# Kernel optimization log

Measured on AMD Instinct MI355X. Metric: run time of the kernel, lower is better.

Reference implementation:

```python
import jax, jax.numpy as jnp
import numpy as np
import math

B, N, D, H = 4, 2048, 256, 4
DH = D // H
EPS = 1e-8


def setup_inputs() -> dict:
    key = jax.random.key(0)
    ks = jax.random.split(key, 8)
    x = jax.random.normal(ks[0], (B, N, D), dtype=jnp.float32)
    # RoPE rotation freqs: exp(i * pos * inv_freq), stored as (cos, sin) pairs -> [N, DH//2, 2]
    d2 = DH // 2
    inv_freq = 1.0 / (10000.0 ** (jnp.arange(d2, dtype=jnp.float32) / d2))
    ang = jnp.arange(N, dtype=jnp.float32)[:, None] * inv_freq[None, :]
    freqs = jnp.stack([jnp.cos(ang), jnp.sin(ang)], axis=-1)  # [N, d2, 2]
    s = 0.02
    g = jnp.ones((D,), dtype=jnp.float32)
    w_qkv = jax.random.normal(ks[1], (D, 3 * D), dtype=jnp.float32) * s
    b_qkv = jnp.zeros((3 * D,), dtype=jnp.float32)
    w_out = jax.random.normal(ks[2], (D, D), dtype=jnp.float32) * s
    b_out = jnp.zeros((D,), dtype=jnp.float32)
    w_gate = jax.random.normal(ks[3], (D, D), dtype=jnp.float32) * s
    b_gate = jnp.zeros((D,), dtype=jnp.float32)
    return {"x": x, "freqs": freqs, "g": g, "w_qkv": w_qkv, "b_qkv": b_qkv,
            "w_out": w_out, "b_out": b_out, "w_gate": w_gate, "b_gate": b_gate}


def _zcrmsnorm(x, g):
    x0 = x - jnp.mean(x, axis=-1, keepdims=True)
    rms = jnp.sqrt(jnp.mean(x0 * x0, axis=-1, keepdims=True) + EPS)
    return x0 / rms * g


def _rope(q, freqs):
    # q: [B,H,N,DH]; freqs: [N,DH//2,2] (cos,sin). Complex multiply on adjacent pairs.
    b, h, n, dh = q.shape
    qp = q.reshape(b, h, n, dh // 2, 2)
    cos = freqs[:n, :, 0][None, None]  # [1,1,N,d2]
    sin = freqs[:n, :, 1][None, None]
    q0, q1 = qp[..., 0], qp[..., 1]
    out = jnp.stack([q0 * cos - q1 * sin, q0 * sin + q1 * cos], axis=-1)
    return out.reshape(b, h, n, dh)


def reference(x, freqs, g, w_qkv, b_qkv, w_out, b_out, w_gate, b_gate):
    b, n, d = x.shape
    h = _zcrmsnorm(x, g)
    qkv = (h @ w_qkv + b_qkv).reshape(b, n, 3, H, DH)
    qkv = jnp.transpose(qkv, (2, 0, 3, 1, 4))  # [3,B,H,N,DH]
    q, k, v = qkv[0], qkv[1], qkv[2]
    q = _rope(q, freqs)
    k = _rope(k, freqs)
    scores = jnp.einsum('bhqd,bhkd->bhqk', q, k) / math.sqrt(DH)
    attn = jax.nn.softmax(scores, axis=-1)  # dropout is identity in eval
    y = jnp.einsum('bhqk,bhkd->bhqd', attn, v)
    y = jnp.transpose(y, (0, 2, 1, 3)).reshape(b, n, d)
    y = y @ w_out + b_out
    gate = jax.nn.sigmoid(h @ w_gate + b_gate)
    return x + gate * y
```

## Files before the change

kernel.cpp:

```cpp
#include <hip/hip_runtime.h>

typedef unsigned short u16;
typedef unsigned int u32;
typedef short short8 __attribute__((ext_vector_type(8)));
typedef float f32x4 __attribute__((ext_vector_type(4)));
typedef float f32x16 __attribute__((ext_vector_type(16)));

#define B_ 4
#define N_ 2048
#define D_ 256
#define H_ 4
#define DH_ 64
#define BN_ 8192

__device__ inline float b2f(u16 u) {
    union { u32 i; float f; } v; v.i = ((u32)u) << 16; return v.f;
}
__device__ inline u16 f2b(float f) {
    union { float f; u32 i; } v; v.f = f;
    return (u16)((v.i + 0x8000u) >> 16);
}
__device__ inline u32 pkbf(float a, float b) {
    union { float f; u32 i; } ua, ub; ua.f = a; ub.f = b;
    return __builtin_amdgcn_perm(ub.i + 0x8000u, ua.i + 0x8000u, 0x07060302u);
}
__device__ inline f32x4 mfma16(short8 a, short8 b, f32x4 c) {
    return __builtin_amdgcn_mfma_f32_16x16x32_bf16(a, b, c, 0, 0, 0);
}
__device__ inline f32x16 mfma32(short8 a, short8 b, f32x16 c) {
    return __builtin_amdgcn_mfma_f32_32x32x16_bf16(a, b, c, 0, 0, 0);
}

__device__ __forceinline__ void gemm_body(
    int bx, int by, int tid,
    const u16* __restrict__ A, const u16* __restrict__ BT,
    const float* __restrict__ bias, void* __restrict__ Cout,
    int Ntot)
{
    const int wave = tid >> 6, lane = tid & 63;
    const int ln15 = lane & 15, quad = lane >> 4;
    const int m0 = bx * 128 + (wave & 1) * 64;
    const int n0 = by * 128 + (wave >> 1) * 64;

    const f32x4 zero = {0.f, 0.f, 0.f, 0.f};
    f32x4 acc[4][4];
    #pragma unroll
    for (int i = 0; i < 4; ++i)
        #pragma unroll
        for (int j = 0; j < 4; ++j) acc[i][j] = zero;

    #pragma unroll
    for (int k0 = 0; k0 < 256; k0 += 32) {
        const int koff = k0 + quad * 8;
        short8 a[4], b[4];
        #pragma unroll
        for (int i = 0; i < 4; ++i)
            a[i] = *(const short8*)(A + (size_t)(m0 + i * 16 + ln15) * 256 + koff);
        #pragma unroll
        for (int j = 0; j < 4; ++j)
            b[j] = *(const short8*)(BT + (size_t)(n0 + j * 16 + ln15) * 256 + koff);
        #pragma unroll
        for (int i = 0; i < 4; ++i)
            #pragma unroll
            for (int j = 0; j < 4; ++j)
                acc[i][j] = mfma16(a[i], b[j], acc[i][j]);
    }

    #pragma unroll
    for (int i = 0; i < 4; ++i) {
        const int r = m0 + i * 16 + quad * 4;
        #pragma unroll
        for (int j = 0; j < 4; ++j) {
            const int c = n0 + j * 16 + ln15;
            const float bv = bias[c];
            #pragma unroll
            for (int rg = 0; rg < 4; ++rg) {
                const size_t idx = (size_t)(r + rg) * Ntot + c;
                ((u16*)Cout)[idx] = f2b(acc[i][j][rg] + bv);
            }
        }
    }
}

__device__ __forceinline__ void gemm_thin_body(
    int bx, int by, int tid,
    const u16* __restrict__ A, const u16* __restrict__ BT,
    const float* __restrict__ bias, void* __restrict__ Cout,
    const float* __restrict__ xin, const u16* __restrict__ gate,
    int mode)
{
    const int wave = tid >> 6, lane = tid & 63;
    const int ln15 = lane & 15, quad = lane >> 4;
    const int m0 = bx * 64 + (wave & 1) * 32;
    const int n0 = by * 64 + (wave >> 1) * 32;

    const f32x4 zero = {0.f, 0.f, 0.f, 0.f};
    f32x4 acc[2][2];
    #pragma unroll
    for (int i = 0; i < 2; ++i)
        #pragma unroll
        for (int j = 0; j < 2; ++j) acc[i][j] = zero;

    #pragma unroll
    for (int k0 = 0; k0 < 256; k0 += 32) {
        const int koff = k0 + quad * 8;
        short8 a[2], b[2];
        #pragma unroll
        for (int i = 0; i < 2; ++i)
            a[i] = *(const short8*)(A + (size_t)(m0 + i * 16 + ln15) * 256 + koff);
        #pragma unroll
        for (int j = 0; j < 2; ++j)
            b[j] = *(const short8*)(BT + (size_t)(n0 + j * 16 + ln15) * 256 + koff);
        #pragma unroll
        for (int i = 0; i < 2; ++i)
            #pragma unroll
            for (int j = 0; j < 2; ++j)
                acc[i][j] = mfma16(a[i], b[j], acc[i][j]);
    }

    #pragma unroll
    for (int i = 0; i < 2; ++i) {
        const int r = m0 + i * 16 + quad * 4;
        #pragma unroll
        for (int j = 0; j < 2; ++j) {
            const int c = n0 + j * 16 + ln15;
            const float bv = bias[c];
            #pragma unroll
            for (int rg = 0; rg < 4; ++rg) {
                const size_t idx = (size_t)(r + rg) * 256 + c;
                float v = acc[i][j][rg] + bv;
                if (mode == 1) {
                    ((u16*)Cout)[idx] = f2b(1.0f / (1.0f + __expf(-v)));
                } else {
                    ((float*)Cout)[idx] = xin[idx] + b2f(gate[idx]) * v;
                }
            }
        }
    }
}

__global__ __launch_bounds__(256) void gemm_ep(
    const u16* __restrict__ A, const u16* __restrict__ BT,
    const float* __restrict__ bias, void* __restrict__ Cout, int Ntot)
{
    gemm_body(blockIdx.x, blockIdx.y, threadIdx.x, A, BT, bias, Cout, Ntot);
}

__global__ __launch_bounds__(256) void gemm_thin(
    const u16* __restrict__ A, const u16* __restrict__ BT,
    const float* __restrict__ bias, void* __restrict__ Cout,
    const float* __restrict__ xin, const u16* __restrict__ gate, int mode)
{
    gemm_thin_body(blockIdx.x, blockIdx.y, threadIdx.x, A, BT, bias, Cout,
                   xin, gate, mode);
}

__global__ __launch_bounds__(256) void norm_transw_k(
    const float* __restrict__ x, const float* __restrict__ g, u16* __restrict__ h,
    const float* __restrict__ wqkv, const float* __restrict__ wout,
    const float* __restrict__ wgate,
    u16* __restrict__ wqkvT, u16* __restrict__ woutT, u16* __restrict__ wgateT)
{
    if (blockIdx.x < 2048) {
        const int wave = threadIdx.x >> 6, lane = threadIdx.x & 63;
        const int t = blockIdx.x * 4 + wave;
        const float4 u = *(const float4*)(x + (size_t)t * D_ + lane * 4);
        float s  = u.x + u.y + u.z + u.w;
        float s2 = u.x * u.x + u.y * u.y + u.z * u.z + u.w * u.w;
        #pragma unroll
        for (int m = 1; m < 64; m <<= 1) {
            s  += __shfl_xor(s, m);
            s2 += __shfl_xor(s2, m);
        }
        float mean = s * (1.0f / D_);
        float var  = s2 * (1.0f / D_) - mean * mean;
        float rinv = rsqrtf(var + 1e-8f);
        const float4 gv = *(const float4*)(g + lane * 4);
        uint2 o;
        o.x = pkbf((u.x - mean) * rinv * gv.x, (u.y - mean) * rinv * gv.y);
        o.y = pkbf((u.z - mean) * rinv * gv.z, (u.w - mean) * rinv * gv.w);
        *(uint2*)(h + (size_t)t * D_ + lane * 4) = o;
    } else {
        int idx = (blockIdx.x - 2048) * 256 + threadIdx.x;
        if (idx < 768 * 256) {
            int nn = idx >> 8, kk = idx & 255;
            wqkvT[idx] = f2b(wqkv[kk * 768 + nn]);
        }
        idx -= 768 * 256;
        if (idx >= 0 && idx < 256 * 256) {
            int nn = idx >> 8, kk = idx & 255;
            woutT[idx]  = f2b(wout[kk * 256 + nn]);
            wgateT[idx] = f2b(wgate[kk * 256 + nn]);
        }
    }
}

#define QSCALE 0.18033688f
__global__ __launch_bounds__(256) void rope_vt_gate_k(
    const u16* __restrict__ qkv, const float* __restrict__ freqs,
    u16* __restrict__ Q, u16* __restrict__ K, u16* __restrict__ VT,
    const u16* __restrict__ h, const u16* __restrict__ wgateT,
    const float* __restrict__ b_gate, u16* __restrict__ gatb)
{
    __shared__ __align__(16) u16 tile[64 * 65];
    const int blk = blockIdx.x;
    if (blk < 1024) {
        const int idx = blk * 256 + threadIdx.x;
        const int t = idx >> 5, rem = idx & 31;
        const int hh = rem >> 3, s8 = rem & 7;
        const int b = t >> 11, n = t & 2047;

        const float4 f0 = *(const float4*)(freqs + (size_t)n * 64 + s8 * 8);
        const float4 f1 = *(const float4*)(freqs + (size_t)n * 64 + s8 * 8 + 4);

        const u16* qp = qkv + (size_t)t * 768 + hh * 64 + s8 * 8;
        const uint4 qv = *(const uint4*)qp;
        const uint4 kv = *(const uint4*)(qp + 256);

        const size_t off = ((size_t)(b * H_ + hh) * N_ + n) * DH_ + s8 * 8;
        uint4 qo, ko;
        {
            float q0 = b2f((u16)(qv.x & 0xffff)), q1 = b2f((u16)(qv.x >> 16));
            float k0 = b2f((u16)(kv.x & 0xffff)), k1 = b2f((u16)(kv.x >> 16));
            qo.x = pkbf((q0 * f0.x - q1 * f0.y) * QSCALE, (q0 * f0.y + q1 * f0.x) * QSCALE);
            ko.x = pkbf(k0 * f0.x - k1 * f0.y, k0 * f0.y + k1 * f0.x);
        }
        {
            float q0 = b2f((u16)(qv.y & 0xffff)), q1 = b2f((u16)(qv.y >> 16));
            float k0 = b2f((u16)(kv.y & 0xffff)), k1 = b2f((u16)(kv.y >> 16));
            qo.y = pkbf((q0 * f0.z - q1 * f0.w) * QSCALE, (q0 * f0.w + q1 * f0.z) * QSCALE);
            ko.y = pkbf(k0 * f0.z - k1 * f0.w, k0 * f0.w + k1 * f0.z);
        }
        {
            float q0 = b2f((u16)(qv.z & 0xffff)), q1 = b2f((u16)(qv.z >> 16));
            float k0 = b2f((u16)(kv.z & 0xffff)), k1 = b2f((u16)(kv.z >> 16));
            qo.z = pkbf((q0 * f1.x - q1 * f1.y) * QSCALE, (q0 * f1.y + q1 * f1.x) * QSCALE);
            ko.z = pkbf(k0 * f1.x - k1 * f1.y, k0 * f1.y + k1 * f1.x);
        }
        {
            float q0 = b2f((u16)(qv.w & 0xffff)), q1 = b2f((u16)(qv.w >> 16));
            float k0 = b2f((u16)(kv.w & 0xffff)), k1 = b2f((u16)(kv.w >> 16));
            qo.w = pkbf((q0 * f1.z - q1 * f1.w) * QSCALE, (q0 * f1.w + q1 * f1.z) * QSCALE);
            ko.w = pkbf(k0 * f1.z - k1 * f1.w, k0 * f1.w + k1 * f1.z);
        }
        *(uint4*)(Q + off) = qo;
        *(uint4*)(K + off) = ko;
    } else if (blk < 1536) {
        const int id2 = blk - 1024;
        const int bh = id2 & 15;
        const int n0 = (id2 >> 4) * 64;
        const int b = bh >> 2, hh = bh & 3;
        #pragma unroll
        for (int rep = 0; rep < 16; ++rep) {
            int idx = rep * 256 + threadIdx.x;
            int nl = idx >> 6, dh = idx & 63;
            tile[dh * 65 + nl] = qkv[(size_t)(b * N_ + n0 + nl) * 768 + 512 + hh * 64 + dh];
        }
        __syncthreads();
        #pragma unroll
        for (int rep = 0; rep < 16; ++rep) {
            int idx = rep * 256 + threadIdx.x;
            int dh = idx >> 6, nl = idx & 63;
            VT[((size_t)bh * 64 + dh) * N_ + n0 + nl] = tile[dh * 65 + nl];
        }
    } else {
        const int id3 = blk - 1536;
        gemm_thin_body(id3 & 127, id3 >> 7, threadIdx.x, h, wgateT, b_gate,
                       (void*)gatb, (const float*)nullptr, (const u16*)nullptr, 1);
    }
}

__global__ __launch_bounds__(256, 2) void attn_k(
    const u16* __restrict__ Q, const u16* __restrict__ K,
    const u16* __restrict__ VT, float* __restrict__ Op,
    float* __restrict__ lvp)
{
    __shared__ __align__(16) u16 Ks[2][64][64];
    __shared__ __align__(16) u16 Vs[2][64][64];
    const int tid = threadIdx.x;
    const int wave = tid >> 6, lane = tid & 63;
    const int l31 = lane & 31, hi = lane >> 5;
    const int id = blockIdx.x;
    const int bh   = ((id & 7) << 1) | ((id >> 3) & 1);
    const int half = (id >> 4) & 1;
    const int q0   = (id >> 5) * 128 + wave * 32;
    const int kt0  = half * 1024;

    const u16* Qh = Q + (size_t)bh * N_ * DH_;
    const u16* Kh = K + (size_t)bh * N_ * DH_;
    const u16* Vh = VT + (size_t)bh * DH_ * N_;

    short8 bq[4];
    #pragma unroll
    for (int kc = 0; kc < 4; ++kc)
        bq[kc] = *(const short8*)(Qh + (size_t)(q0 + l31) * DH_ + kc * 16 + hi * 8);

    f32x16 o0, o1;
    #pragma unroll
    for (int i = 0; i < 16; ++i) { o0[i] = 0.f; o1[i] = 0.f; }
    float lv = 0.f;

    const int srow = tid >> 2, sq4 = tid & 3;
    const int sw = srow & 7;
    const int wg0 = ((sq4) ^ sw) * 8;
    const int wg1 = ((sq4 + 4) ^ sw) * 8;
    const int rsw = l31 & 7;

    {
        uint4 k0 = *(const uint4*)(Kh + (size_t)(kt0 + srow) * DH_ + sq4 * 8);
        uint4 k1 = *(const uint4*)(Kh + (size_t)(kt0 + srow) * DH_ + (sq4 + 4) * 8);
        uint4 v0 = *(const uint4*)(Vh + (size_t)srow * N_ + kt0 + sq4 * 8);
        uint4 v1 = *(const uint4*)(Vh + (size_t)srow * N_ + kt0 + (sq4 + 4) * 8);
        *(uint4*)&Ks[0][srow][wg0] = k0;
        *(uint4*)&Ks[0][srow][wg1] = k1;
        *(uint4*)&Vs[0][srow][wg0] = v0;
        *(uint4*)&Vs[0][srow][wg1] = v1;
    }
    __syncthreads();

    int p = 0;
    for (int c = 0; c < 16; ++c) {
        const bool more = (c + 1 < 16);
        uint4 k0, k1, v0, v1;
        if (more) {
            const int ktn = kt0 + (c + 1) * 64;
            k0 = *(const uint4*)(Kh + (size_t)(ktn + srow) * DH_ + sq4 * 8);
            k1 = *(const uint4*)(Kh + (size_t)(ktn + srow) * DH_ + (sq4 + 4) * 8);
            v0 = *(const uint4*)(Vh + (size_t)srow * N_ + ktn + sq4 * 8);
            v1 = *(const uint4*)(Vh + (size_t)srow * N_ + ktn + (sq4 + 4) * 8);
        }

        f32x16 st0, st1;
        #pragma unroll
        for (int i = 0; i < 16; ++i) { st0[i] = 0.f; st1[i] = 0.f; }
        #pragma unroll
        for (int kc = 0; kc < 4; ++kc) {
            const int gran = ((2 * kc + hi) ^ rsw) * 8;
            short8 ka0 = *(const short8*)&Ks[p][l31][gran];
            short8 ka1 = *(const short8*)&Ks[p][32 + l31][gran];
            st0 = mfma32(ka0, bq[kc], st0);
            st1 = mfma32(ka1, bq[kc], st1);
        }

        short8 pb[4];
        #pragma unroll
        for (int g = 0; g < 2; ++g) {
            float pr[16];
            #pragma unroll
            for (int r = 0; r < 16; ++r) {
                pr[r] = exp2f(g ? st1[r] : st0[r]);
                lv += pr[r];
            }
            #pragma unroll
            for (int kc2 = 0; kc2 < 2; ++kc2) {
                u32 X0, X1, Y0, Y1;
                asm("v_cvt_pk_bf16_f32 %0, %1, %2" : "=v"(X0) : "v"(pr[8*kc2+0]), "v"(pr[8*kc2+1]));
                asm("v_cvt_pk_bf16_f32 %0, %1, %2" : "=v"(X1) : "v"(pr[8*kc2+2]), "v"(pr[8*kc2+3]));
                asm("v_cvt_pk_bf16_f32 %0, %1, %2" : "=v"(Y0) : "v"(pr[8*kc2+4]), "v"(pr[8*kc2+5]));
                asm("v_cvt_pk_bf16_f32 %0, %1, %2" : "=v"(Y1) : "v"(pr[8*kc2+6]), "v"(pr[8*kc2+7]));
                asm("v_permlane32_swap_b32 %0, %1" : "+v"(X0), "+v"(Y0));
                asm("v_permlane32_swap_b32 %0, %1" : "+v"(X1), "+v"(Y1));
                union { u32 u[4]; short8 s; } bf;
                bf.u[0] = X0; bf.u[1] = X1; bf.u[2] = Y0; bf.u[3] = Y1;
                pb[g * 2 + kc2] = bf.s;
            }
        }

        #pragma unroll
        for (int kc = 0; kc < 4; ++kc) {
            const int gran = ((2 * kc + hi) ^ rsw) * 8;
            short8 va0 = *(const short8*)&Vs[p][l31][gran];
            short8 va1 = *(const short8*)&Vs[p][32 + l31][gran];
            o0 = mfma32(va0, pb[kc], o0);
            o1 = mfma32(va1, pb[kc], o1);
        }

        if (more) {
            *(uint4*)&Ks[p ^ 1][srow][wg0] = k0;
            *(uint4*)&Ks[p ^ 1][srow][wg1] = k1;
            *(uint4*)&Vs[p ^ 1][srow][wg0] = v0;
            *(uint4*)&Vs[p ^ 1][srow][wg1] = v1;
        }
        __syncthreads();
        p ^= 1;
    }

    lv += __shfl_xor(lv, 32);
    const size_t rowo = ((size_t)(half * 16 + bh) * N_ + q0 + l31) * DH_;
    #pragma unroll
    for (int go = 0; go < 2; ++go) {
        #pragma unroll
        for (int rq = 0; rq < 4; ++rq) {
            float4 w4;
            if (go == 0) {
                w4.x = o0[rq*4+0]; w4.y = o0[rq*4+1]; w4.z = o0[rq*4+2]; w4.w = o0[rq*4+3];
            } else {
                w4.x = o1[rq*4+0]; w4.y = o1[rq*4+1]; w4.z = o1[rq*4+2]; w4.w = o1[rq*4+3];
            }
            *(float4*)(Op + rowo + go * 32 + 8 * rq + 4 * hi) = w4;
        }
    }
    if (hi == 0) lvp[(size_t)(half * 16 + bh) * N_ + q0 + l31] = lv;
}

__global__ __launch_bounds__(256) void combine_k(
    const float* __restrict__ Op, const float* __restrict__ lvp,
    u16* __restrict__ yt)
{
    const int t = blockIdx.x * 256 + threadIdx.x;
    const int dh0 = (t & 7) * 8;
    const int q   = (t >> 3) & 2047;
    const int bh  = t >> 14;
    const size_t o0 = ((size_t)bh * N_ + q) * DH_ + dh0;
    const size_t o1 = o0 + (size_t)16 * N_ * DH_;
    const float4 a0 = *(const float4*)(Op + o0);
    const float4 a1 = *(const float4*)(Op + o0 + 4);
    const float4 c0 = *(const float4*)(Op + o1);
    const float4 c1 = *(const float4*)(Op + o1 + 4);
    const float rl = 1.0f / (lvp[(size_t)bh * N_ + q] + lvp[(size_t)(16 + bh) * N_ + q]);
    uint4 w;
    w.x = pkbf((a0.x + c0.x) * rl, (a0.y + c0.y) * rl);
    w.y = pkbf((a0.z + c0.z) * rl, (a0.w + c0.w) * rl);
    w.z = pkbf((a1.x + c1.x) * rl, (a1.y + c1.y) * rl);
    w.w = pkbf((a1.z + c1.z) * rl, (a1.w + c1.w) * rl);
    const int b = bh >> 2, h = bh & 3;
    *(uint4*)(yt + ((size_t)b * N_ + q) * D_ + h * 64 + dh0) = w;
}

extern "C" void kernel_launch(void* const* d_in, const int* in_sizes, int n_in,
                              void* d_out, int out_size, void* d_ws, size_t ws_size,
                              hipStream_t stream) {
    const float* x      = (const float*)d_in[0];
    const float* freqs  = (const float*)d_in[1];
    const float* g      = (const float*)d_in[2];
    const float* w_qkv  = (const float*)d_in[3];
    const float* b_qkv  = (const float*)d_in[4];
    const float* w_out  = (const float*)d_in[5];
    const float* b_out  = (const float*)d_in[6];
    const float* w_gate = (const float*)d_in[7];
    const float* b_gate = (const float*)d_in[8];
    float* out = (float*)d_out;

    char* ws = (char*)d_ws;
    size_t off = 0;
    auto carve = [&](size_t nelem) -> u16* {
        u16* p = (u16*)(ws + off);
        off += ((nelem * 2 + 255) / 256) * 256;
        return p;
    };
    u16* h      = carve((size_t)BN_ * D_);
    u16* qkv    = carve((size_t)BN_ * 768);
    u16* Qb     = carve((size_t)BN_ * D_);
    u16* Kb     = carve((size_t)BN_ * D_);
    u16* VT     = carve((size_t)BN_ * D_);
    u16* gatb   = carve((size_t)BN_ * D_);
    u16* wqkvT  = carve((size_t)768 * 256);
    u16* woutT  = carve((size_t)256 * 256);
    u16* wgateT = carve((size_t)256 * 256);
    float* Op  = (float*)ws;
    float* lvp = (float*)wqkvT;
    u16*   yt  = Qb;

    hipLaunchKernelGGL(norm_transw_k, dim3(3072), dim3(256), 0, stream,
                       x, g, h, w_qkv, w_out, w_gate, wqkvT, woutT, wgateT);
    hipLaunchKernelGGL(gemm_ep, dim3(BN_ / 128, 6), dim3(256), 0, stream,
                       h, wqkvT, b_qkv, (void*)qkv, 768);
    hipLaunchKernelGGL(rope_vt_gate_k, dim3(2048), dim3(256), 0, stream,
                       qkv, freqs, Qb, Kb, VT, h, wgateT, b_gate, gatb);
    hipLaunchKernelGGL(attn_k, dim3(512), dim3(256), 0, stream,
                       Qb, Kb, VT, Op, lvp);
    hipLaunchKernelGGL(combine_k, dim3(1024), dim3(256), 0, stream,
                       Op, lvp, yt);
    hipLaunchKernelGGL(gemm_thin, dim3(128, 4), dim3(256), 0, stream,
                       yt, woutT, b_out, (void*)out, x, gatb, 2);
}
```

Before: 166.8 us.

## Split attention KV range into four partitions and interleave QK/PV per half-tile

The attention kernel now splits each head's key range into four 512-key partitions instead of two, doubling the grid to 1024 blocks. It also raises the launch-bounds occupancy hint from 2 to 4. The score computation is restructured to process one 32-key half at a time, feeding each half's probabilities straight into the PV MFMAs, which cuts live registers. The combine kernel sums four partial outputs, and dedicated workspace buffers hold the larger partials. The aim is more parallelism and occupancy, at the cost of extra partial-output traffic and reduction work.

```diff
diff --git a/kernel.cpp b/kernel.cpp
--- a/kernel.cpp
+++ b/kernel.cpp
@@ -270,7 +270,7 @@
     }
 }
 
-__global__ __launch_bounds__(256, 2) void attn_k(
+__global__ __launch_bounds__(256, 4) void attn_k(
     const u16* __restrict__ Q, const u16* __restrict__ K,
     const u16* __restrict__ VT, float* __restrict__ Op,
     float* __restrict__ lvp)
@@ -282,9 +282,9 @@
     const int l31 = lane & 31, hi = lane >> 5;
     const int id = blockIdx.x;
     const int bh   = ((id & 7) << 1) | ((id >> 3) & 1);
-    const int half = (id >> 4) & 1;
-    const int q0   = (id >> 5) * 128 + wave * 32;
-    const int kt0  = half * 1024;
+    const int quar = (id >> 4) & 3;
+    const int q0   = (id >> 6) * 128 + wave * 32;
+    const int kt0  = quar * 512;
 
     const u16* Qh = Q + (size_t)bh * N_ * DH_;
     const u16* Kh = K + (size_t)bh * N_ * DH_;
@@ -319,8 +319,8 @@
     __syncthreads();
 
     int p = 0;
-    for (int c = 0; c < 16; ++c) {
-        const bool more = (c + 1 < 16);
+    for (int c = 0; c < 8; ++c) {
+        const bool more = (c + 1 < 8);
         uint4 k0, k1, v0, v1;
         if (more) {
             const int ktn = kt0 + (c + 1) * 64;
@@ -330,49 +330,39 @@
             v1 = *(const uint4*)(Vh + (size_t)srow * N_ + ktn + (sq4 + 4) * 8);
         }
 
-        f32x16 st0, st1;
-        #pragma unroll
-        for (int i = 0; i < 16; ++i) { st0[i] = 0.f; st1[i] = 0.f; }
-        #pragma unroll
-        for (int kc = 0; kc < 4; ++kc) {
-            const int gran = ((2 * kc + hi) ^ rsw) * 8;
-            short8 ka0 = *(const short8*)&Ks[p][l31][gran];
-            short8 ka1 = *(const short8*)&Ks[p][32 + l31][gran];
-            st0 = mfma32(ka0, bq[kc], st0);
-            st1 = mfma32(ka1, bq[kc], st1);
-        }
-
-        short8 pb[4];
         #pragma unroll
         for (int g = 0; g < 2; ++g) {
-            float pr[16];
+            f32x16 st;
+            #pragma unroll
+            for (int i = 0; i < 16; ++i) st[i] = 0.f;
+            #pragma unroll
+            for (int kc = 0; kc < 4; ++kc) {
+                const int gran = ((2 * kc + hi) ^ rsw) * 8;
+                short8 ka = *(const short8*)&Ks[p][g * 32 + l31][gran];
+                st = mfma32(ka, bq[kc], st);
+            }
             #pragma unroll
             for (int r = 0; r < 16; ++r) {
-                pr[r] = exp2f(g ? st1[r] : st0[r]);
-                lv += pr[r];
+                st[r] = exp2f(st[r]);
+                lv += st[r];
             }
             #pragma unroll
             for (int kc2 = 0; kc2 < 2; ++kc2) {
                 u32 X0, X1, Y0, Y1;
-                asm("v_cvt_pk_bf16_f32 %0, %1, %2" : "=v"(X0) : "v"(pr[8*kc2+0]), "v"(pr[8*kc2+1]));
-                asm("v_cvt_pk_bf16_f32 %0, %1, %2" : "=v"(X1) : "v"(pr[8*kc2+2]), "v"(pr[8*kc2+3]));
-                asm("v_cvt_pk_bf16_f32 %0, %1, %2" : "=v"(Y0) : "v"(pr[8*kc2+4]), "v"(pr[8*kc2+5]));
-                asm("v_cvt_pk_bf16_f32 %0, %1, %2" : "=v"(Y1) : "v"(pr[8*kc2+6]), "v"(pr[8*kc2+7]));
+                asm("v_cvt_pk_bf16_f32 %0, %1, %2" : "=v"(X0) : "v"(st[8*kc2+0]), "v"(st[8*kc2+1]));
+                asm("v_cvt_pk_bf16_f32 %0, %1, %2" : "=v"(X1) : "v"(st[8*kc2+2]), "v"(st[8*kc2+3]));
+                asm("v_cvt_pk_bf16_f32 %0, %1, %2" : "=v"(Y0) : "v"(st[8*kc2+4]), "v"(st[8*kc2+5]));
+                asm("v_cvt_pk_bf16_f32 %0, %1, %2" : "=v"(Y1) : "v"(st[8*kc2+6]), "v"(st[8*kc2+7]));
                 asm("v_permlane32_swap_b32 %0, %1" : "+v"(X0), "+v"(Y0));
                 asm("v_permlane32_swap_b32 %0, %1" : "+v"(X1), "+v"(Y1));
                 union { u32 u[4]; short8 s; } bf;
                 bf.u[0] = X0; bf.u[1] = X1; bf.u[2] = Y0; bf.u[3] = Y1;
-                pb[g * 2 + kc2] = bf.s;
-            }
-        }
-
-        #pragma unroll
-        for (int kc = 0; kc < 4; ++kc) {
-            const int gran = ((2 * kc + hi) ^ rsw) * 8;
-            short8 va0 = *(const short8*)&Vs[p][l31][gran];
-            short8 va1 = *(const short8*)&Vs[p][32 + l31][gran];
-            o0 = mfma32(va0, pb[kc], o0);
-            o1 = mfma32(va1, pb[kc], o1);
+                const int gran = ((2 * (2 * g + kc2) + hi) ^ rsw) * 8;
+                short8 va0 = *(const short8*)&Vs[p][l31][gran];
+                short8 va1 = *(const short8*)&Vs[p][32 + l31][gran];
+                o0 = mfma32(va0, bf.s, o0);
+                o1 = mfma32(va1, bf.s, o1);
+            }
         }
 
         if (more) {
@@ -386,7 +376,7 @@
     }
 
     lv += __shfl_xor(lv, 32);
-    const size_t rowo = ((size_t)(half * 16 + bh) * N_ + q0 + l31) * DH_;
+    const size_t rowo = ((size_t)(quar * 16 + bh) * N_ + q0 + l31) * DH_;
     #pragma unroll
     for (int go = 0; go < 2; ++go) {
         #pragma unroll
@@ -400,7 +390,7 @@
             *(float4*)(Op + rowo + go * 32 + 8 * rq + 4 * hi) = w4;
         }
     }
-    if (hi == 0) lvp[(size_t)(half * 16 + bh) * N_ + q0 + l31] = lv;
+    if (hi == 0) lvp[(size_t)(quar * 16 + bh) * N_ + q0 + l31] = lv;
 }
 
 __global__ __launch_bounds__(256) void combine_k(
@@ -411,18 +401,25 @@
     const int dh0 = (t & 7) * 8;
     const int q   = (t >> 3) & 2047;
     const int bh  = t >> 14;
-    const size_t o0 = ((size_t)bh * N_ + q) * DH_ + dh0;
-    const size_t o1 = o0 + (size_t)16 * N_ * DH_;
-    const float4 a0 = *(const float4*)(Op + o0);
-    const float4 a1 = *(const float4*)(Op + o0 + 4);
-    const float4 c0 = *(const float4*)(Op + o1);
-    const float4 c1 = *(const float4*)(Op + o1 + 4);
-    const float rl = 1.0f / (lvp[(size_t)bh * N_ + q] + lvp[(size_t)(16 + bh) * N_ + q]);
+    float a[8];
+    #pragma unroll
+    for (int i = 0; i < 8; ++i) a[i] = 0.f;
+    float lsum = 0.f;
+    #pragma unroll
+    for (int pp = 0; pp < 4; ++pp) {
+        const size_t o0 = ((size_t)(pp * 16 + bh) * N_ + q) * DH_ + dh0;
+        const float4 u0 = *(const float4*)(Op + o0);
+        const float4 u1 = *(const float4*)(Op + o0 + 4);
+        a[0] += u0.x; a[1] += u0.y; a[2] += u0.z; a[3] += u0.w;
+        a[4] += u1.x; a[5] += u1.y; a[6] += u1.z; a[7] += u1.w;
+        lsum += lvp[(size_t)(pp * 16 + bh) * N_ + q];
+    }
+    const float rl = 1.0f / lsum;
     uint4 w;
-    w.x = pkbf((a0.x + c0.x) * rl, (a0.y + c0.y) * rl);
-    w.y = pkbf((a0.z + c0.z) * rl, (a0.w + c0.w) * rl);
-    w.z = pkbf((a1.x + c1.x) * rl, (a1.y + c1.y) * rl);
-    w.w = pkbf((a1.z + c1.z) * rl, (a1.w + c1.w) * rl);
+    w.x = pkbf(a[0] * rl, a[1] * rl);
+    w.y = pkbf(a[2] * rl, a[3] * rl);
+    w.z = pkbf(a[4] * rl, a[5] * rl);
+    w.w = pkbf(a[6] * rl, a[7] * rl);
     const int b = bh >> 2, h = bh & 3;
     *(uint4*)(yt + ((size_t)b * N_ + q) * D_ + h * 64 + dh0) = w;
 }
@@ -457,8 +454,8 @@
     u16* wqkvT  = carve((size_t)768 * 256);
     u16* woutT  = carve((size_t)256 * 256);
     u16* wgateT = carve((size_t)256 * 256);
-    float* Op  = (float*)ws;
-    float* lvp = (float*)wqkvT;
+    float* Op  = (float*)carve((size_t)4 * 16 * N_ * DH_ * 2);
+    float* lvp = (float*)carve((size_t)4 * 16 * N_ * 2);
     u16*   yt  = Qb;
 
     hipLaunchKernelGGL(norm_transw_k, dim3(3072), dim3(256), 0, stream,
@@ -467,7 +464,7 @@
                        h, wqkvT, b_qkv, (void*)qkv, 768);
     hipLaunchKernelGGL(rope_vt_gate_k, dim3(2048), dim3(256), 0, stream,
                        qkv, freqs, Qb, Kb, VT, h, wgateT, b_gate, gatb);
-    hipLaunchKernelGGL(attn_k, dim3(512), dim3(256), 0, stream,
+    hipLaunchKernelGGL(attn_k, dim3(1024), dim3(256), 0, stream,
                        Qb, Kb, VT, Op, lvp);
     hipLaunchKernelGGL(combine_k, dim3(1024), dim3(256), 0, stream,
                        Op, lvp, yt);
```

Measured after the change: 162.2 us. -2.7%, faster.
